# Optimization experiments

Hardware: AMD Instinct MI355X
Metric: run time of the kernel (lower is better)

The kernel has to match this reference:

```python
import jax, jax.numpy as jnp
import numpy as np

W, HN, C, NHEAD = 256, 128, 512, 8


def layer_norm(x, w, b, eps=1e-5):
    m = x.mean(-1, keepdims=True)
    v = ((x - m) ** 2).mean(-1, keepdims=True)
    return (x - m) / jnp.sqrt(v + eps) * w + b


def setup_inputs() -> dict:
    key = jax.random.key(0)
    ks = jax.random.split(key, 6)
    s = 0.02
    return {
        "feat_left": jax.random.normal(ks[0], (W, HN, C), jnp.float32),
        "feat_right": jax.random.normal(ks[1], (W, HN, C), jnp.float32),
        "pos": jax.random.normal(ks[2], (2 * W - 1, C), jnp.float32),
        "pos_indexes": jax.random.randint(ks[3], (W * W,), 0, 2 * W - 1, dtype=jnp.int32),
        "ln_w": jnp.ones((C,), jnp.float32),
        "ln_b": jnp.zeros((C,), jnp.float32),
        "in_proj_w": jax.random.normal(ks[4], (3 * C, C), jnp.float32) * s,
        "in_proj_b": jnp.zeros((3 * C,), jnp.float32),
        "out_w": jax.random.normal(ks[5], (C, C), jnp.float32) * s,
        "out_b": jnp.zeros((C,), jnp.float32),
    }


def reference(feat_left, feat_right, pos, pos_indexes, ln_w, ln_b, in_proj_w, in_proj_b, out_w, out_b):
    w, n, c = feat_left.shape
    e = NHEAD
    hd = c // e
    scaling = hd ** -0.5

    # pre-norm (same norm1 applied to both streams)
    ql = layer_norm(feat_left, ln_w, ln_b)     # [W,N,C]
    kv_in = layer_norm(feat_right, ln_w, ln_b)  # [W,N,C]

    # cross-attn projections: q from left with in_proj[:C], k/v from right with in_proj[C:]
    q = ql @ in_proj_w[:c].T + in_proj_b[:c]
    kv = kv_in @ in_proj_w[c:].T + in_proj_b[c:]
    k, v = jnp.split(kv, 2, axis=-1)

    # relative pos encoding gather: [2W-1,C] -> [W*W,C] -> [W,W',C]
    pe = pos[pos_indexes].reshape(w, w, c)
    qr_kr = pe @ in_proj_w[: 2 * c].T + in_proj_b[: 2 * c]
    q_r, k_r = jnp.split(qr_kr, 2, axis=-1)

    q = (q * scaling).reshape(w, n, e, hd)
    q_r = (q_r * scaling).reshape(w, w, e, hd)
    k = k.reshape(w, n, e, hd)
    v = v.reshape(w, n, e, hd)
    k_r = k_r.reshape(w, w, e, hd)

    # content-content + content-pos + pos-content scores: [N,E,W,W']
    attn = (jnp.einsum('wnec,vnec->newv', q, k)
            + jnp.einsum('wnec,wvec->newv', q, k_r)
            + jnp.einsum('vnec,wvec->newv', k, q_r))

    raw_attn = attn.sum(axis=1)                      # [N,W,W']
    p = jax.nn.softmax(attn, axis=-1)
    v_o = jnp.einsum('newv,vnec->wnec', p, v).reshape(w, n, c)
    v_o = v_o @ out_w.T + out_b

    return feat_left + v_o, raw_attn
```

## Files before the change

### kernel.cpp

```cpp
#include <hip/hip_runtime.h>

#define WW 256
#define NB 128
#define CD 512
#define NE 8
#define HD 64
#define NCHUNKS 4
#define SCALING 0.125f

typedef __attribute__((ext_vector_type(8))) short bfx8;
typedef __attribute__((ext_vector_type(4))) float fx4;

#define OFF_MEAN   0u
#define OFF_RSTD   65536u
#define OFF_WPB    131072u
#define OFF_OWB    524288u
#define OFF_S      655360u
#define OFF_U      656896u
#define OFF_PQ     658432u
#define OFF_PK     789504u
#define OFF_QB     920576u
#define OFF_KB     9309184u
#define OFF_VB     17697792u
#define OFF_ATTN   26086400u
#define OFF_T3     42863616u
#define OFF_PB     51252224u
#define OFF_VOB    59640832u

__device__ __forceinline__ unsigned short f2bf(float f) {
  unsigned u = __builtin_bit_cast(unsigned, f);
  u = (u + 0x7fffu + ((u >> 16) & 1u)) >> 16;
  return (unsigned short)u;
}
__device__ __forceinline__ float bf2f(unsigned short h) {
  unsigned u = ((unsigned)h) << 16;
  return __builtin_bit_cast(float, u);
}

#define GLDS16(g, l)                                                          \
  __builtin_amdgcn_global_load_lds(                                           \
      (const __attribute__((address_space(1))) void*)(g),                     \
      (__attribute__((address_space(3))) void*)(l), 16, 0, 0)

__global__ __launch_bounds__(256) void cvt_kernel(const float* __restrict__ a,
                                                  unsigned short* __restrict__ b,
                                                  int n8) {
  int i = blockIdx.x * 256 + threadIdx.x;
  if (i >= n8) return;
  float4 x = ((const float4*)a)[2 * i];
  float4 y = ((const float4*)a)[2 * i + 1];
  int4 o;
  o.x = (int)(((unsigned)f2bf(x.y) << 16) | f2bf(x.x));
  o.y = (int)(((unsigned)f2bf(x.w) << 16) | f2bf(x.z));
  o.z = (int)(((unsigned)f2bf(y.y) << 16) | f2bf(y.x));
  o.w = (int)(((unsigned)f2bf(y.w) << 16) | f2bf(y.z));
  ((int4*)b)[i] = o;
}

__global__ __launch_bounds__(256) void stats_kernel(const float* __restrict__ L,
                                                    const float* __restrict__ R,
                                                    float* __restrict__ mean,
                                                    float* __restrict__ rstd,
                                                    unsigned short* __restrict__ flb,
                                                    unsigned short* __restrict__ frb) {
  int wave = threadIdx.x >> 6, lane = threadIdx.x & 63;
  int row = blockIdx.x * 4 + wave;
  const float* src = (row < 32768) ? (L + (size_t)row * CD) : (R + (size_t)(row - 32768) * CD);
  unsigned short* drow = (row < 32768) ? (flb + (size_t)row * CD) : (frb + (size_t)(row - 32768) * CD);
  float4 a = *(const float4*)(src + lane * 4);
  float4 b = *(const float4*)(src + 256 + lane * 4);
  short4 sa, sb;
  sa.x = (short)f2bf(a.x); sa.y = (short)f2bf(a.y); sa.z = (short)f2bf(a.z); sa.w = (short)f2bf(a.w);
  sb.x = (short)f2bf(b.x); sb.y = (short)f2bf(b.y); sb.z = (short)f2bf(b.z); sb.w = (short)f2bf(b.w);
  *(short4*)(drow + lane * 4) = sa;
  *(short4*)(drow + 256 + lane * 4) = sb;
  float s  = a.x + a.y + a.z + a.w + b.x + b.y + b.z + b.w;
  float ss = a.x*a.x + a.y*a.y + a.z*a.z + a.w*a.w + b.x*b.x + b.y*b.y + b.z*b.z + b.w*b.w;
#pragma unroll
  for (int off = 32; off > 0; off >>= 1) {
    s  += __shfl_xor(s, off);
    ss += __shfl_xor(ss, off);
  }
  if (lane == 0) {
    float m = s * (1.0f / 512.0f);
    float v = ss * (1.0f / 512.0f) - m * m;
    mean[row] = m;
    rstd[row] = rsqrtf(v + 1e-5f);
  }
}

__global__ __launch_bounds__(256) void prep_kernel(const float* __restrict__ ipw,
                                                   const float* __restrict__ ipb,
                                                   const float* __restrict__ lnw,
                                                   const float* __restrict__ lnb,
                                                   unsigned short* __restrict__ Wpb,
                                                   float* __restrict__ S,
                                                   float* __restrict__ U) {
  int o = blockIdx.x, t = threadIdx.x;
  float s = 0.f, u = 0.f;
#pragma unroll
  for (int j0 = 0; j0 < 512; j0 += 256) {
    int j = j0 + t;
    float w0 = ipw[(size_t)o * 512 + j];
    float wl = w0 * lnw[j];
    unsigned short h = f2bf(wl);
    Wpb[(size_t)o * 512 + j] = h;
    s += bf2f(h);
    u += w0 * lnb[j];
  }
  __shared__ float rs[4], ru[4];
  int lane = t & 63, wv = t >> 6;
#pragma unroll
  for (int off = 32; off > 0; off >>= 1) { s += __shfl_xor(s, off); u += __shfl_xor(u, off); }
  if (lane == 0) { rs[wv] = s; ru[wv] = u; }
  __syncthreads();
  if (t == 0) {
    S[o] = rs[0] + rs[1] + rs[2] + rs[3];
    U[o] = ru[0] + ru[1] + ru[2] + ru[3] + ipb[o];
  }
}

__global__ __launch_bounds__(256) void gemm_ln(const unsigned short* __restrict__ A,
                                               const unsigned short* __restrict__ Bw,
                                               const float* __restrict__ S,
                                               const float* __restrict__ U,
                                               const float* __restrict__ mean,
                                               const float* __restrict__ rstd,
                                               unsigned short* __restrict__ out0,
                                               unsigned short* __restrict__ out1,
                                               int wOff, int statOff, float scale) {
  __shared__ unsigned short As[2][128 * 32];
  __shared__ unsigned short Bs[2][128 * 32];
  int t = threadIdx.x;
  int lane = t & 63, w = t >> 6;
  int quad = lane >> 4, l15 = lane & 15;
  int wm = w >> 1, wn = w & 1;
  int m0 = blockIdx.x * 128, n0 = blockIdx.y * 128;

  int cs = ((lane & 3) ^ ((lane >> 3) & 3)) * 8;
  unsigned lo0 = (unsigned)(w * 16) * 32;
  unsigned lo1 = (unsigned)(64 + w * 16) * 32;
  const unsigned short* gA0 = A + (size_t)(m0 + w * 16 + (lane >> 2)) * 512 + cs;
  const unsigned short* gA1 = gA0 + (size_t)64 * 512;
  const unsigned short* gB0 = Bw + (size_t)(wOff + n0 + w * 16 + (lane >> 2)) * 512 + cs;
  const unsigned short* gB1 = gB0 + (size_t)64 * 512;

  fx4 acc[4][4];
#pragma unroll
  for (int i = 0; i < 4; ++i)
#pragma unroll
    for (int j = 0; j < 4; ++j) acc[i][j] = (fx4){0.f, 0.f, 0.f, 0.f};

  int ro = (quad ^ ((l15 >> 1) & 3)) * 8;

#define STAGE_G(buf, kk)                                                      \
  do {                                                                        \
    GLDS16(gA0 + (kk), &As[buf][lo0]);                                        \
    GLDS16(gA1 + (kk), &As[buf][lo1]);                                        \
    GLDS16(gB0 + (kk), &Bs[buf][lo0]);                                        \
    GLDS16(gB1 + (kk), &Bs[buf][lo1]);                                        \
  } while (0)

#define COMPUTE_G(buf)                                                        \
  do {                                                                        \
    const unsigned short* Ab = &As[buf][0];                                   \
    const unsigned short* Bb = &Bs[buf][0];                                   \
    bfx8 af[4], bfr[4];                                                       \
    _Pragma("unroll")                                                         \
    for (int i = 0; i < 4; ++i)                                               \
      af[i] = *(const bfx8*)(Ab + (size_t)(wm * 64 + i * 16 + l15) * 32 + ro);\
    _Pragma("unroll")                                                         \
    for (int j = 0; j < 4; ++j)                                               \
      bfr[j] = *(const bfx8*)(Bb + (size_t)(wn * 64 + j * 16 + l15) * 32 + ro);\
    _Pragma("unroll")                                                         \
    for (int i = 0; i < 4; ++i)                                               \
      _Pragma("unroll")                                                       \
      for (int j = 0; j < 4; ++j)                                             \
        acc[i][j] = __builtin_amdgcn_mfma_f32_16x16x32_bf16(af[i], bfr[j], acc[i][j], 0, 0, 0); \
  } while (0)

  STAGE_G(0, 0);
  int cur = 0;
  for (int kt = 0; kt < 480; kt += 32) {
    STAGE_G(cur ^ 1, kt + 32);
    asm volatile("s_waitcnt vmcnt(4)" ::: "memory");
    __builtin_amdgcn_s_barrier();
    __builtin_amdgcn_sched_barrier(0);
    COMPUTE_G(cur);
    asm volatile("s_waitcnt lgkmcnt(0)" ::: "memory");
    __builtin_amdgcn_s_barrier();
    __builtin_amdgcn_sched_barrier(0);
    cur ^= 1;
  }
  asm volatile("s_waitcnt vmcnt(0)" ::: "memory");
  __builtin_amdgcn_s_barrier();
  __builtin_amdgcn_sched_barrier(0);
  COMPUTE_G(cur);

  float mn[16], rs[16];
#pragma unroll
  for (int i = 0; i < 4; ++i)
#pragma unroll
    for (int r = 0; r < 4; ++r) {
      int m = statOff + m0 + wm * 64 + i * 16 + quad * 4 + r;
      mn[i * 4 + r] = mean[m];
      rs[i * 4 + r] = rstd[m];
    }
#pragma unroll
  for (int j = 0; j < 4; ++j) {
    int oc = n0 + wn * 64 + j * 16 + l15;
    int o = wOff + oc;
    float Sv = S[o], Uv = U[o];
    unsigned short* dst; int cc;
    if (oc < 512) { dst = out0; cc = oc; } else { dst = out1; cc = oc - 512; }
#pragma unroll
    for (int i = 0; i < 4; ++i)
#pragma unroll
      for (int r = 0; r < 4; ++r) {
        int m = m0 + wm * 64 + i * 16 + quad * 4 + r;
        dst[(size_t)m * 512 + cc] =
            f2bf(((acc[i][j][r] - mn[i * 4 + r] * Sv) * rs[i * 4 + r] + Uv) * scale);
      }
  }
#undef STAGE_G
#undef COMPUTE_G
}

__global__ __launch_bounds__(256) void gemm_out(const unsigned short* __restrict__ A,
                                                const unsigned short* __restrict__ Bw,
                                                const float* __restrict__ ob,
                                                const float* __restrict__ fl,
                                                float* __restrict__ out, int wc) {
  __shared__ unsigned short As[2][128 * 32];
  __shared__ unsigned short Bs[2][128 * 32];
  int t = threadIdx.x;
  int lane = t & 63, w = t >> 6;
  int quad = lane >> 4, l15 = lane & 15;
  int wm = w >> 1, wn = w & 1;
  int n0 = blockIdx.x * 128, m0 = blockIdx.y * 128;

  int cs = ((lane & 3) ^ ((lane >> 3) & 3)) * 8;
  unsigned lo0 = (unsigned)(w * 16) * 32;
  unsigned lo1 = (unsigned)(64 + w * 16) * 32;
  const unsigned short* gA0 = A + (size_t)(m0 + w * 16 + (lane >> 2)) * 512 + cs;
  const unsigned short* gA1 = gA0 + (size_t)64 * 512;
  const unsigned short* gB0 = Bw + (size_t)(n0 + w * 16 + (lane >> 2)) * 512 + cs;
  const unsigned short* gB1 = gB0 + (size_t)64 * 512;

  fx4 acc[4][4];
#pragma unroll
  for (int i = 0; i < 4; ++i)
#pragma unroll
    for (int j = 0; j < 4; ++j) acc[i][j] = (fx4){0.f, 0.f, 0.f, 0.f};

  int ro = (quad ^ ((l15 >> 1) & 3)) * 8;

#define STAGE_O(buf, kk)                                                      \
  do {                                                                        \
    GLDS16(gA0 + (kk), &As[buf][lo0]);                                        \
    GLDS16(gA1 + (kk), &As[buf][lo1]);                                        \
    GLDS16(gB0 + (kk), &Bs[buf][lo0]);                                        \
    GLDS16(gB1 + (kk), &Bs[buf][lo1]);                                        \
  } while (0)

#define COMPUTE_O(buf)                                                        \
  do {                                                                        \
    const unsigned short* Ab = &As[buf][0];                                   \
    const unsigned short* Bb = &Bs[buf][0];                                   \
    bfx8 af[4], bfr[4];                                                       \
    _Pragma("unroll")                                                         \
    for (int i = 0; i < 4; ++i)                                               \
      af[i] = *(const bfx8*)(Ab + (size_t)(wm * 64 + i * 16 + l15) * 32 + ro);\
    _Pragma("unroll")                                                         \
    for (int j = 0; j < 4; ++j)                                               \
      bfr[j] = *(const bfx8*)(Bb + (size_t)(wn * 64 + j * 16 + l15) * 32 + ro);\
    _Pragma("unroll")                                                         \
    for (int i = 0; i < 4; ++i)                                               \
      _Pragma("unroll")                                                       \
      for (int j = 0; j < 4; ++j)                                             \
        acc[i][j] = __builtin_amdgcn_mfma_f32_16x16x32_bf16(af[i], bfr[j], acc[i][j], 0, 0, 0); \
  } while (0)

  STAGE_O(0, 0);
  int cur = 0;
  for (int kt = 0; kt < 480; kt += 32) {
    STAGE_O(cur ^ 1, kt + 32);
    asm volatile("s_waitcnt vmcnt(4)" ::: "memory");
    __builtin_amdgcn_s_barrier();
    __builtin_amdgcn_sched_barrier(0);
    COMPUTE_O(cur);
    asm volatile("s_waitcnt lgkmcnt(0)" ::: "memory");
    __builtin_amdgcn_s_barrier();
    __builtin_amdgcn_sched_barrier(0);
    cur ^= 1;
  }
  asm volatile("s_waitcnt vmcnt(0)" ::: "memory");
  __builtin_amdgcn_s_barrier();
  __builtin_amdgcn_sched_barrier(0);
  COMPUTE_O(cur);

  size_t gbase = (size_t)wc * 64 * NB * CD;
#pragma unroll
  for (int j = 0; j < 4; ++j) {
    int o = n0 + wn * 64 + j * 16 + l15;
    float bias = ob[o];
#pragma unroll
    for (int i = 0; i < 4; ++i)
#pragma unroll
      for (int r = 0; r < 4; ++r) {
        int m = m0 + wm * 64 + i * 16 + quad * 4 + r;
        size_t go = gbase + (size_t)m * 512 + o;
        out[go] = acc[i][j][r] + bias + fl[go];
      }
  }
#undef STAGE_O
#undef COMPUTE_O
}

__global__ __launch_bounds__(256) void posproj_mfma(const unsigned short* __restrict__ Apos,
                                                    const unsigned short* __restrict__ Bw,
                                                    const float* __restrict__ ipb,
                                                    unsigned short* __restrict__ Pq,
                                                    unsigned short* __restrict__ Pk) {
  __shared__ unsigned short As[2][128 * 32];
  __shared__ unsigned short Bs[2][128 * 32];
  int t = threadIdx.x;
  int lane = t & 63, w = t >> 6;
  int quad = lane >> 4, l15 = lane & 15;
  int wm = w >> 1, wn = w & 1;
  int m0 = blockIdx.x * 128, n0 = blockIdx.y * 128;

  int cs = ((lane & 3) ^ ((lane >> 3) & 3)) * 8;
  unsigned lo0 = (unsigned)(w * 16) * 32;
  unsigned lo1 = (unsigned)(64 + w * 16) * 32;
  int ar0 = m0 + w * 16 + (lane >> 2); if (ar0 > 510) ar0 = 510;
  int ar1 = m0 + 64 + w * 16 + (lane >> 2); if (ar1 > 510) ar1 = 510;
  const unsigned short* gA0 = Apos + (size_t)ar0 * 512 + cs;
  const unsigned short* gA1 = Apos + (size_t)ar1 * 512 + cs;
  const unsigned short* gB0 = Bw + (size_t)(n0 + w * 16 + (lane >> 2)) * 512 + cs;
  const unsigned short* gB1 = gB0 + (size_t)64 * 512;

  fx4 acc[4][4];
#pragma unroll
  for (int i = 0; i < 4; ++i)
#pragma unroll
    for (int j = 0; j < 4; ++j) acc[i][j] = (fx4){0.f, 0.f, 0.f, 0.f};

  int ro = (quad ^ ((l15 >> 1) & 3)) * 8;

#define STAGE_P(buf, kk)                                                      \
  do {                                                                        \
    GLDS16(gA0 + (kk), &As[buf][lo0]);                                        \
    GLDS16(gA1 + (kk), &As[buf][lo1]);                                        \
    GLDS16(gB0 + (kk), &Bs[buf][lo0]);                                        \
    GLDS16(gB1 + (kk), &Bs[buf][lo1]);                                        \
  } while (0)

#define COMPUTE_P(buf)                                                        \
  do {                                                                        \
    const unsigned short* Ab = &As[buf][0];                                   \
    const unsigned short* Bb = &Bs[buf][0];                                   \
    bfx8 af[4], bfr[4];                                                       \
    _Pragma("unroll")                                                         \
    for (int i = 0; i < 4; ++i)                                               \
      af[i] = *(const bfx8*)(Ab + (size_t)(wm * 64 + i * 16 + l15) * 32 + ro);\
    _Pragma("unroll")                                                         \
    for (int j = 0; j < 4; ++j)                                               \
      bfr[j] = *(const bfx8*)(Bb + (size_t)(wn * 64 + j * 16 + l15) * 32 + ro);\
    _Pragma("unroll")                                                         \
    for (int i = 0; i < 4; ++i)                                               \
      _Pragma("unroll")                                                       \
      for (int j = 0; j < 4; ++j)                                             \
        acc[i][j] = __builtin_amdgcn_mfma_f32_16x16x32_bf16(af[i], bfr[j], acc[i][j], 0, 0, 0); \
  } while (0)

  STAGE_P(0, 0);
  int cur = 0;
  for (int kt = 0; kt < 480; kt += 32) {
    STAGE_P(cur ^ 1, kt + 32);
    asm volatile("s_waitcnt vmcnt(4)" ::: "memory");
    __builtin_amdgcn_s_barrier();
    __builtin_amdgcn_sched_barrier(0);
    COMPUTE_P(cur);
    asm volatile("s_waitcnt lgkmcnt(0)" ::: "memory");
    __builtin_amdgcn_s_barrier();
    __builtin_amdgcn_sched_barrier(0);
    cur ^= 1;
  }
  asm volatile("s_waitcnt vmcnt(0)" ::: "memory");
  __builtin_amdgcn_s_barrier();
  __builtin_amdgcn_sched_barrier(0);
  COMPUTE_P(cur);

#pragma unroll
  for (int j = 0; j < 4; ++j) {
    int o = n0 + wn * 64 + j * 16 + l15;
    float bias = ipb[o];
    float scale = (o < 512) ? SCALING : 1.0f;
    unsigned short* dst; int cc;
    if (o < 512) { dst = Pq; cc = o; } else { dst = Pk; cc = o - 512; }
#pragma unroll
    for (int i = 0; i < 4; ++i)
#pragma unroll
      for (int r = 0; r < 4; ++r) {
        int m = m0 + wm * 64 + i * 16 + quad * 4 + r;
        if (m < 511)
          dst[(size_t)m * 512 + cc] = f2bf((acc[i][j][r] + bias) * scale);
      }
  }
#undef STAGE_P
#undef COMPUTE_P
}

__global__ __launch_bounds__(256) void t3_kernel(const unsigned short* __restrict__ kb,
                                                 const unsigned short* __restrict__ Pq,
                                                 const int* __restrict__ idx,
                                                 unsigned short* __restrict__ T3, int wc) {
  __shared__ unsigned short As[128 * 72];
  __shared__ unsigned short Bs[64 * 72];
  int t = threadIdx.x, lane = t & 63, w = t >> 6;
  int quad = lane >> 4, l15 = lane & 15;
  int e = blockIdx.x, v = blockIdx.y;
  const unsigned short* asrc = kb + ((size_t)v * NB) * 512 + e * 64;
  for (int c = t; c < 1024; c += 256) {
    int row = c >> 3, c8 = c & 7;
    *(int4*)(As + row * 72 + c8 * 8) = *(const int4*)(asrc + (size_t)row * 512 + c8 * 8);
  }
  for (int c = t; c < 512; c += 256) {
    int row = c >> 3, c8 = c & 7;
    int ri = idx[(wc * 64 + row) * WW + v];
    *(int4*)(Bs + row * 72 + c8 * 8) = *(const int4*)(Pq + (size_t)ri * 512 + e * 64 + c8 * 8);
  }
  __syncthreads();
  fx4 acc[2][4];
#pragma unroll
  for (int i = 0; i < 2; ++i)
#pragma unroll
    for (int j = 0; j < 4; ++j) acc[i][j] = (fx4){0.f, 0.f, 0.f, 0.f};
#pragma unroll
  for (int kt = 0; kt < 64; kt += 32) {
    bfx8 af[2], bfr[4];
#pragma unroll
    for (int i = 0; i < 2; ++i)
      af[i] = *(const bfx8*)(As + (w * 32 + i * 16 + l15) * 72 + kt + quad * 8);
#pragma unroll
    for (int j = 0; j < 4; ++j)
      bfr[j] = *(const bfx8*)(Bs + (j * 16 + l15) * 72 + kt + quad * 8);
#pragma unroll
    for (int i = 0; i < 2; ++i)
#pragma unroll
      for (int j = 0; j < 4; ++j)
        acc[i][j] = __builtin_amdgcn_mfma_f32_16x16x32_bf16(af[i], bfr[j], acc[i][j], 0, 0, 0);
  }
#pragma unroll
  for (int i = 0; i < 2; ++i)
#pragma unroll
    for (int j = 0; j < 4; ++j)
#pragma unroll
      for (int r = 0; r < 4; ++r) {
        int n = w * 32 + i * 16 + quad * 4 + r;
        int wq = j * 16 + l15;
        T3[(((size_t)e * WW + v) * NB + n) * 64 + wq] = f2bf(acc[i][j][r]);
      }
}

__global__ __launch_bounds__(256) void t1_kernel(const unsigned short* __restrict__ qb,
                                                 const unsigned short* __restrict__ kb,
                                                 const unsigned short* __restrict__ T3,
                                                 float* __restrict__ attn, int wc) {
  __shared__ unsigned short As[64 * 72];
  __shared__ unsigned short Bs[256 * 72];
  int t = threadIdx.x, lane = t & 63, w = t >> 6;
  int quad = lane >> 4, l15 = lane & 15;
  int e = blockIdx.x, n = blockIdx.y;
  const unsigned short* asrc = qb + ((size_t)(wc * 64) * NB + n) * 512 + e * 64;
  for (int c = t; c < 512; c += 256) {
    int row = c >> 3, c8 = c & 7;
    *(int4*)(As + row * 72 + c8 * 8) = *(const int4*)(asrc + (size_t)row * NB * 512 + c8 * 8);
  }
  const unsigned short* bsrc = kb + (size_t)n * 512 + e * 64;
  for (int c = t; c < 2048; c += 256) {
    int row = c >> 3, c8 = c & 7;
    *(int4*)(Bs + row * 72 + c8 * 8) = *(const int4*)(bsrc + (size_t)row * NB * 512 + c8 * 8);
  }
  __syncthreads();
  fx4 acc[4][4];
#pragma unroll
  for (int i = 0; i < 4; ++i)
#pragma unroll
    for (int j = 0; j < 4; ++j) acc[i][j] = (fx4){0.f, 0.f, 0.f, 0.f};
#pragma unroll
  for (int kt = 0; kt < 64; kt += 32) {
    bfx8 af[4], bfr[4];
#pragma unroll
    for (int i = 0; i < 4; ++i)
      af[i] = *(const bfx8*)(As + (i * 16 + l15) * 72 + kt + quad * 8);
#pragma unroll
    for (int j = 0; j < 4; ++j)
      bfr[j] = *(const bfx8*)(Bs + (w * 64 + j * 16 + l15) * 72 + kt + quad * 8);
#pragma unroll
    for (int i = 0; i < 4; ++i)
#pragma unroll
      for (int j = 0; j < 4; ++j)
        acc[i][j] = __builtin_amdgcn_mfma_f32_16x16x32_bf16(af[i], bfr[j], acc[i][j], 0, 0, 0);
  }
  __syncthreads();
  const unsigned short* tsrc = T3 + ((size_t)e * WW * NB + n) * 64;
  for (int c = t; c < 2048; c += 256) {
    int row = c >> 3, c8 = c & 7;
    *(int4*)(Bs + row * 72 + c8 * 8) = *(const int4*)(tsrc + (size_t)row * NB * 64 + c8 * 8);
  }
  __syncthreads();
#pragma unroll
  for (int i = 0; i < 4; ++i)
#pragma unroll
    for (int j = 0; j < 4; ++j) {
      int vg = w * 64 + j * 16 + l15;
      ushort4 t3v = *(const ushort4*)(Bs + (size_t)vg * 72 + i * 16 + quad * 4);
      const unsigned short tv[4] = {t3v.x, t3v.y, t3v.z, t3v.w};
#pragma unroll
      for (int r = 0; r < 4; ++r) {
        int wq = i * 16 + quad * 4 + r;
        float* p = attn + (((size_t)n * NE + e) * 64 + wq) * WW + vg;
        *p = acc[i][j][r] + bf2f(tv[r]);
      }
    }
}

__global__ __launch_bounds__(256) void t2s_kernel(const unsigned short* __restrict__ qb,
                                                  const unsigned short* __restrict__ Pk,
                                                  const int* __restrict__ idx,
                                                  const float* __restrict__ attn,
                                                  unsigned short* __restrict__ pbuf,
                                                  float* __restrict__ raw, int wc) {
  __shared__ unsigned short As[16 * 72];
  __shared__ unsigned short Bs[256 * 72];
  __shared__ int idxs[256];
  __shared__ float redm[16 * 4];
  __shared__ float reds[16 * 4];
  int t = threadIdx.x, lane = t & 63, w = t >> 6;
  int quad = lane >> 4, l15 = lane & 15;
  int wq = blockIdx.x, nt = blockIdx.y;
  int n0 = nt * 16;
  idxs[t] = idx[((size_t)(wc * 64 + wq)) * WW + t];

  fx4 raws[4];
#pragma unroll
  for (int j = 0; j < 4; ++j) raws[j] = (fx4){0.f, 0.f, 0.f, 0.f};

  const unsigned short* abase = qb + ((size_t)(wc * 64 + wq) * NB + n0) * 512;

  for (int e = 0; e < NE; ++e) {
    __syncthreads();
    if (t < 128) {
      int row = t >> 3, c8 = t & 7;
      *(int4*)(As + row * 72 + c8 * 8) = *(const int4*)(abase + (size_t)row * 512 + e * 64 + c8 * 8);
    }
    for (int c = t; c < 2048; c += 256) {
      int row = c >> 3, c8 = c & 7;
      int ri = idxs[row];
      *(int4*)(Bs + row * 72 + c8 * 8) = *(const int4*)(Pk + (size_t)ri * 512 + e * 64 + c8 * 8);
    }
    __syncthreads();

    fx4 acc[4];
#pragma unroll
    for (int j = 0; j < 4; ++j) acc[j] = (fx4){0.f, 0.f, 0.f, 0.f};
    bfx8 af0 = *(const bfx8*)(As + l15 * 72 + quad * 8);
    bfx8 af1 = *(const bfx8*)(As + l15 * 72 + 32 + quad * 8);
#pragma unroll
    for (int j = 0; j < 4; ++j) {
      bfx8 b0 = *(const bfx8*)(Bs + (w * 64 + j * 16 + l15) * 72 + quad * 8);
      acc[j] = __builtin_amdgcn_mfma_f32_16x16x32_bf16(af0, b0, acc[j], 0, 0, 0);
    }
#pragma unroll
    for (int j = 0; j < 4; ++j) {
      bfx8 b1 = *(const bfx8*)(Bs + (w * 64 + j * 16 + l15) * 72 + 32 + quad * 8);
      acc[j] = __builtin_amdgcn_mfma_f32_16x16x32_bf16(af1, b1, acc[j], 0, 0, 0);
    }

#pragma unroll
    for (int j = 0; j < 4; ++j) {
      int vg = w * 64 + j * 16 + l15;
#pragma unroll
      for (int r = 0; r < 4; ++r) {
        int n = n0 + quad * 4 + r;
        acc[j][r] += attn[(((size_t)n * NE + e) * 64 + wq) * WW + vg];
      }
    }

    float rm[4];
#pragma unroll
    for (int r = 0; r < 4; ++r)
      rm[r] = fmaxf(fmaxf(acc[0][r], acc[1][r]), fmaxf(acc[2][r], acc[3][r]));
#pragma unroll
    for (int off = 1; off < 16; off <<= 1)
#pragma unroll
      for (int r = 0; r < 4; ++r) rm[r] = fmaxf(rm[r], __shfl_xor(rm[r], off));
    if (l15 == 0) {
#pragma unroll
      for (int r = 0; r < 4; ++r) redm[(quad * 4 + r) * 4 + w] = rm[r];
    }
    __syncthreads();
    float fm[4];
#pragma unroll
    for (int r = 0; r < 4; ++r) {
      const float* rp = redm + (quad * 4 + r) * 4;
      fm[r] = fmaxf(fmaxf(rp[0], rp[1]), fmaxf(rp[2], rp[3]));
    }
    float ex[4][4];
    float ls[4] = {0.f, 0.f, 0.f, 0.f};
#pragma unroll
    for (int j = 0; j < 4; ++j)
#pragma unroll
      for (int r = 0; r < 4; ++r) {
        ex[j][r] = __expf(acc[j][r] - fm[r]);
        ls[r] += ex[j][r];
      }
#pragma unroll
    for (int off = 1; off < 16; off <<= 1)
#pragma unroll
      for (int r = 0; r < 4; ++r) ls[r] += __shfl_xor(ls[r], off);
    if (l15 == 0) {
#pragma unroll
      for (int r = 0; r < 4; ++r) reds[(quad * 4 + r) * 4 + w] = ls[r];
    }
    __syncthreads();
    float inv[4];
#pragma unroll
    for (int r = 0; r < 4; ++r) {
      const float* sp = reds + (quad * 4 + r) * 4;
      inv[r] = 1.0f / (sp[0] + sp[1] + sp[2] + sp[3]);
    }
#pragma unroll
    for (int j = 0; j < 4; ++j) {
      int vg = w * 64 + j * 16 + l15;
#pragma unroll
      for (int r = 0; r < 4; ++r) {
        int n = n0 + quad * 4 + r;
        pbuf[(((size_t)n * NE + e) * 64 + wq) * WW + vg] = f2bf(ex[j][r] * inv[r]);
        raws[j][r] += acc[j][r];
      }
    }
  }

#pragma unroll
  for (int j = 0; j < 4; ++j) {
    int vg = w * 64 + j * 16 + l15;
#pragma unroll
    for (int r = 0; r < 4; ++r) {
      int n = n0 + quad * 4 + r;
      raw[((size_t)n * WW + wc * 64 + wq) * WW + vg] = raws[j][r];
    }
  }
}

__global__ __launch_bounds__(256) void pv_kernel(const unsigned short* __restrict__ pb,
                                                 const unsigned short* __restrict__ vb,
                                                 unsigned short* __restrict__ vob) {
  __shared__ unsigned short As[64 * 72];
  __shared__ unsigned short Bs[64 * 72];
  int t = threadIdx.x, lane = t & 63, w = t >> 6;
  int quad = lane >> 4, l15 = lane & 15;
  int e = blockIdx.x, n = blockIdx.y;
  fx4 acc[4];
#pragma unroll
  for (int j = 0; j < 4; ++j) acc[j] = (fx4){0.f, 0.f, 0.f, 0.f};
  const unsigned short* abase = pb + (((size_t)n * NE + e) * 64) * WW;
  for (int kc = 0; kc < 4; ++kc) {
    for (int c = t; c < 512; c += 256) {
      int row = c >> 3, c8 = c & 7;
      *(int4*)(As + row * 72 + c8 * 8) = *(const int4*)(abase + (size_t)row * WW + kc * 64 + c8 * 8);
    }
    for (int c = t; c < 512; c += 256) {
      int row = c >> 3, c8 = c & 7;
      *(int4*)(Bs + row * 72 + c8 * 8) =
          *(const int4*)(vb + ((size_t)(kc * 64 + row) * NB + n) * 512 + e * 64 + c8 * 8);
    }
    __syncthreads();
#pragma unroll
    for (int kt = 0; kt < 64; kt += 32) {
      bfx8 af = *(const bfx8*)(As + (w * 16 + l15) * 72 + kt + quad * 8);
      bfx8 bfr[4];
#pragma unroll
      for (int j = 0; j < 4; ++j)
        bfr[j] = *(const bfx8*)(Bs + (j * 16 + l15) * 72 + kt + quad * 8);
#pragma unroll
      for (int j = 0; j < 4; ++j)
        acc[j] = __builtin_amdgcn_mfma_f32_16x16x32_bf16(af, bfr[j], acc[j], 0, 0, 0);
    }
    __syncthreads();
  }
#pragma unroll
  for (int j = 0; j < 4; ++j)
#pragma unroll
    for (int r = 0; r < 4; ++r) {
      int wq = w * 16 + quad * 4 + r;
      vob[((size_t)wq * NB + n) * 512 + e * 64 + j * 16 + l15] = f2bf(acc[j][r]);
    }
}

extern "C" void kernel_launch(void* const* d_in, const int* in_sizes, int n_in,
                              void* d_out, int out_size, void* d_ws, size_t ws_size,
                              hipStream_t stream) {
  const float* fl  = (const float*)d_in[0];
  const float* fr  = (const float*)d_in[1];
  const float* pos = (const float*)d_in[2];
  const int*  pidx = (const int*)d_in[3];
  const float* lnw = (const float*)d_in[4];
  const float* lnb = (const float*)d_in[5];
  const float* ipw = (const float*)d_in[6];
  const float* ipb = (const float*)d_in[7];
  const float* ow  = (const float*)d_in[8];
  const float* ob  = (const float*)d_in[9];

  float* ws   = (float*)d_ws;
  float* mean = ws + OFF_MEAN;
  float* rstd = ws + OFF_RSTD;
  unsigned short* Wpb = (unsigned short*)(ws + OFF_WPB);
  unsigned short* owb = (unsigned short*)(ws + OFF_OWB);
  float* S    = ws + OFF_S;
  float* U    = ws + OFF_U;
  unsigned short* Pq = (unsigned short*)(ws + OFF_PQ);
  unsigned short* Pk = (unsigned short*)(ws + OFF_PK);
  unsigned short* qb = (unsigned short*)(ws + OFF_QB);
  unsigned short* kb = (unsigned short*)(ws + OFF_KB);
  unsigned short* vb = (unsigned short*)(ws + OFF_VB);
  float* attn = ws + OFF_ATTN;
  unsigned short* T3  = (unsigned short*)(ws + OFF_T3);
  unsigned short* pb  = (unsigned short*)(ws + OFF_PB);
  unsigned short* vob = (unsigned short*)(ws + OFF_VOB);
  unsigned short* flb = (unsigned short*)(ws + OFF_ATTN);
  unsigned short* frb = flb + (size_t)32768 * 512;
  unsigned short* posb = (unsigned short*)(ws + OFF_T3);
  unsigned short* ipwb = posb + 262144;

  float* outF = (float*)d_out;
  float* outR = outF + (size_t)WW * NB * CD;

  stats_kernel<<<16384, 256, 0, stream>>>(fl, fr, mean, rstd, flb, frb);
  prep_kernel<<<1536, 256, 0, stream>>>(ipw, ipb, lnw, lnb, Wpb, S, U);
  cvt_kernel<<<128, 256, 0, stream>>>(ow, owb, 32768);
  cvt_kernel<<<128, 256, 0, stream>>>(pos, posb, 32704);
  cvt_kernel<<<256, 256, 0, stream>>>(ipw, ipwb, 65536);
  posproj_mfma<<<dim3(4, 8), 256, 0, stream>>>(posb, ipwb, ipb, Pq, Pk);
  gemm_ln<<<dim3(256, 4), 256, 0, stream>>>(flb, Wpb, S, U, mean, rstd, qb, qb, 0, 0, SCALING);
  gemm_ln<<<dim3(256, 8), 256, 0, stream>>>(frb, Wpb, S, U, mean, rstd, kb, vb, 512, 32768, 1.0f);

  for (int wc = 0; wc < NCHUNKS; ++wc) {
    t3_kernel<<<dim3(8, 256), 256, 0, stream>>>(kb, Pq, pidx, T3, wc);
    t1_kernel<<<dim3(8, 128), 256, 0, stream>>>(qb, kb, T3, attn, wc);
    t2s_kernel<<<dim3(64, 8), 256, 0, stream>>>(qb, Pk, pidx, attn, pb, outR, wc);
    pv_kernel<<<dim3(8, 128), 256, 0, stream>>>(pb, vb, vob);
    gemm_out<<<dim3(4, 64), 256, 0, stream>>>(vob, owb, ob, fl, outF, wc);
  }
}
```

Measured before the change: 825.0 us.

## Store partial attention scores in bf16, batch output GEMM, process four rows per wave in stats

The intermediate content-plus-position score buffer is now written and read as bf16 instead of fp32, which halves its traffic between t1 and t2s. The per-chunk output projection is replaced by one gemm_out launch over all chunks, with pv results accumulated into a full-size buffer placed after the bf16 attention buffer. The stats kernel now handles four rows per wave so that several loads are in flight at once, and launches fewer blocks. Rounding the pre-softmax scores to bf16 adds precision loss.

```diff
diff --git a/kernel.cpp b/kernel.cpp
--- a/kernel.cpp
+++ b/kernel.cpp
@@ -25,7 +25,6 @@
 #define OFF_ATTN   26086400u
 #define OFF_T3     42863616u
 #define OFF_PB     51252224u
-#define OFF_VOB    59640832u
 
 __device__ __forceinline__ unsigned short f2bf(float f) {
   unsigned u = __builtin_bit_cast(unsigned, f);
@@ -64,28 +63,47 @@
                                                     unsigned short* __restrict__ flb,
                                                     unsigned short* __restrict__ frb) {
   int wave = threadIdx.x >> 6, lane = threadIdx.x & 63;
-  int row = blockIdx.x * 4 + wave;
-  const float* src = (row < 32768) ? (L + (size_t)row * CD) : (R + (size_t)(row - 32768) * CD);
-  unsigned short* drow = (row < 32768) ? (flb + (size_t)row * CD) : (frb + (size_t)(row - 32768) * CD);
-  float4 a = *(const float4*)(src + lane * 4);
-  float4 b = *(const float4*)(src + 256 + lane * 4);
-  short4 sa, sb;
-  sa.x = (short)f2bf(a.x); sa.y = (short)f2bf(a.y); sa.z = (short)f2bf(a.z); sa.w = (short)f2bf(a.w);
-  sb.x = (short)f2bf(b.x); sb.y = (short)f2bf(b.y); sb.z = (short)f2bf(b.z); sb.w = (short)f2bf(b.w);
-  *(short4*)(drow + lane * 4) = sa;
-  *(short4*)(drow + 256 + lane * 4) = sb;
-  float s  = a.x + a.y + a.z + a.w + b.x + b.y + b.z + b.w;
-  float ss = a.x*a.x + a.y*a.y + a.z*a.z + a.w*a.w + b.x*b.x + b.y*b.y + b.z*b.z + b.w*b.w;
-#pragma unroll
-  for (int off = 32; off > 0; off >>= 1) {
-    s  += __shfl_xor(s, off);
-    ss += __shfl_xor(ss, off);
-  }
+  int base = (blockIdx.x * 4 + wave) * 4;
+  float4 a[4], b[4];
+#pragma unroll
+  for (int r = 0; r < 4; ++r) {
+    int row = base + r;
+    const float* src = (row < 32768) ? (L + (size_t)row * CD) : (R + (size_t)(row - 32768) * CD);
+    a[r] = *(const float4*)(src + lane * 4);
+    b[r] = *(const float4*)(src + 256 + lane * 4);
+  }
+#pragma unroll
+  for (int r = 0; r < 4; ++r) {
+    int row = base + r;
+    unsigned short* drow = (row < 32768) ? (flb + (size_t)row * CD) : (frb + (size_t)(row - 32768) * CD);
+    short4 sa, sb;
+    sa.x = (short)f2bf(a[r].x); sa.y = (short)f2bf(a[r].y); sa.z = (short)f2bf(a[r].z); sa.w = (short)f2bf(a[r].w);
+    sb.x = (short)f2bf(b[r].x); sb.y = (short)f2bf(b[r].y); sb.z = (short)f2bf(b[r].z); sb.w = (short)f2bf(b[r].w);
+    *(short4*)(drow + lane * 4) = sa;
+    *(short4*)(drow + 256 + lane * 4) = sb;
+  }
+  float s[4], ss[4];
+#pragma unroll
+  for (int r = 0; r < 4; ++r) {
+    s[r]  = a[r].x + a[r].y + a[r].z + a[r].w + b[r].x + b[r].y + b[r].z + b[r].w;
+    ss[r] = a[r].x*a[r].x + a[r].y*a[r].y + a[r].z*a[r].z + a[r].w*a[r].w
+          + b[r].x*b[r].x + b[r].y*b[r].y + b[r].z*b[r].z + b[r].w*b[r].w;
+  }
+#pragma unroll
+  for (int off = 32; off > 0; off >>= 1)
+#pragma unroll
+    for (int r = 0; r < 4; ++r) {
+      s[r]  += __shfl_xor(s[r], off);
+      ss[r] += __shfl_xor(ss[r], off);
+    }
   if (lane == 0) {
-    float m = s * (1.0f / 512.0f);
-    float v = ss * (1.0f / 512.0f) - m * m;
-    mean[row] = m;
-    rstd[row] = rsqrtf(v + 1e-5f);
+#pragma unroll
+    for (int r = 0; r < 4; ++r) {
+      float m = s[r] * (1.0f / 512.0f);
+      float v = ss[r] * (1.0f / 512.0f) - m * m;
+      mean[base + r] = m;
+      rstd[base + r] = rsqrtf(v + 1e-5f);
+    }
   }
 }
 
@@ -230,7 +248,7 @@
                                                 const unsigned short* __restrict__ Bw,
                                                 const float* __restrict__ ob,
                                                 const float* __restrict__ fl,
-                                                float* __restrict__ out, int wc) {
+                                                float* __restrict__ out) {
   __shared__ unsigned short As[2][128 * 32];
   __shared__ unsigned short Bs[2][128 * 32];
   int t = threadIdx.x;
@@ -299,7 +317,6 @@
   __builtin_amdgcn_sched_barrier(0);
   COMPUTE_O(cur);
 
-  size_t gbase = (size_t)wc * 64 * NB * CD;
 #pragma unroll
   for (int j = 0; j < 4; ++j) {
     int o = n0 + wn * 64 + j * 16 + l15;
@@ -309,7 +326,7 @@
 #pragma unroll
       for (int r = 0; r < 4; ++r) {
         int m = m0 + wm * 64 + i * 16 + quad * 4 + r;
-        size_t go = gbase + (size_t)m * 512 + o;
+        size_t go = (size_t)m * 512 + o;
         out[go] = acc[i][j][r] + bias + fl[go];
       }
   }
@@ -467,7 +484,7 @@
 __global__ __launch_bounds__(256) void t1_kernel(const unsigned short* __restrict__ qb,
                                                  const unsigned short* __restrict__ kb,
                                                  const unsigned short* __restrict__ T3,
-                                                 float* __restrict__ attn, int wc) {
+                                                 unsigned short* __restrict__ attnb, int wc) {
   __shared__ unsigned short As[64 * 72];
   __shared__ unsigned short Bs[256 * 72];
   int t = threadIdx.x, lane = t & 63, w = t >> 6;
@@ -521,8 +538,7 @@
 #pragma unroll
       for (int r = 0; r < 4; ++r) {
         int wq = i * 16 + quad * 4 + r;
-        float* p = attn + (((size_t)n * NE + e) * 64 + wq) * WW + vg;
-        *p = acc[i][j][r] + bf2f(tv[r]);
+        attnb[(((size_t)n * NE + e) * 64 + wq) * WW + vg] = f2bf(acc[i][j][r] + bf2f(tv[r]));
       }
     }
 }
@@ -530,7 +546,7 @@
 __global__ __launch_bounds__(256) void t2s_kernel(const unsigned short* __restrict__ qb,
                                                   const unsigned short* __restrict__ Pk,
                                                   const int* __restrict__ idx,
-                                                  const float* __restrict__ attn,
+                                                  const unsigned short* __restrict__ attnb,
                                                   unsigned short* __restrict__ pbuf,
                                                   float* __restrict__ raw, int wc) {
   __shared__ unsigned short As[16 * 72];
@@ -585,7 +601,7 @@
 #pragma unroll
       for (int r = 0; r < 4; ++r) {
         int n = n0 + quad * 4 + r;
-        acc[j][r] += attn[(((size_t)n * NE + e) * 64 + wq) * WW + vg];
+        acc[j][r] += bf2f(attnb[(((size_t)n * NE + e) * 64 + wq) * WW + vg]);
       }
     }
 
@@ -726,10 +742,10 @@
   unsigned short* qb = (unsigned short*)(ws + OFF_QB);
   unsigned short* kb = (unsigned short*)(ws + OFF_KB);
   unsigned short* vb = (unsigned short*)(ws + OFF_VB);
-  float* attn = ws + OFF_ATTN;
+  unsigned short* attnb = (unsigned short*)(ws + OFF_ATTN);
+  unsigned short* vob4  = attnb + (size_t)16777216;
   unsigned short* T3  = (unsigned short*)(ws + OFF_T3);
   unsigned short* pb  = (unsigned short*)(ws + OFF_PB);
-  unsigned short* vob = (unsigned short*)(ws + OFF_VOB);
   unsigned short* flb = (unsigned short*)(ws + OFF_ATTN);
   unsigned short* frb = flb + (size_t)32768 * 512;
   unsigned short* posb = (unsigned short*)(ws + OFF_T3);
@@ -738,7 +754,7 @@
   float* outF = (float*)d_out;
   float* outR = outF + (size_t)WW * NB * CD;
 
-  stats_kernel<<<16384, 256, 0, stream>>>(fl, fr, mean, rstd, flb, frb);
+  stats_kernel<<<4096, 256, 0, stream>>>(fl, fr, mean, rstd, flb, frb);
   prep_kernel<<<1536, 256, 0, stream>>>(ipw, ipb, lnw, lnb, Wpb, S, U);
   cvt_kernel<<<128, 256, 0, stream>>>(ow, owb, 32768);
   cvt_kernel<<<128, 256, 0, stream>>>(pos, posb, 32704);
@@ -749,9 +765,9 @@
 
   for (int wc = 0; wc < NCHUNKS; ++wc) {
     t3_kernel<<<dim3(8, 256), 256, 0, stream>>>(kb, Pq, pidx, T3, wc);
-    t1_kernel<<<dim3(8, 128), 256, 0, stream>>>(qb, kb, T3, attn, wc);
-    t2s_kernel<<<dim3(64, 8), 256, 0, stream>>>(qb, Pk, pidx, attn, pb, outR, wc);
-    pv_kernel<<<dim3(8, 128), 256, 0, stream>>>(pb, vb, vob);
-    gemm_out<<<dim3(4, 64), 256, 0, stream>>>(vob, owb, ob, fl, outF, wc);
-  }
-}
+    t1_kernel<<<dim3(8, 128), 256, 0, stream>>>(qb, kb, T3, attnb, wc);
+    t2s_kernel<<<dim3(64, 8), 256, 0, stream>>>(qb, Pk, pidx, attnb, pb, outR, wc);
+    pv_kernel<<<dim3(8, 128), 256, 0, stream>>>(pb, vb, vob4 + (size_t)wc * 64 * NB * 512);
+  }
+  gemm_out<<<dim3(4, 256), 256, 0, stream>>>(vob4, owb, ob, fl, outF);
+}
```

Result: faster. 770.4 us (-6.6%).
